# Optimization experiments

Measured on AMD Instinct MI355X. Metric: run time of the kernel, lower is better.

## Reference

```python
import jax, jax.numpy as jnp
import numpy as np

NEG_SLOPE = 0.2  # PyG GATConv default leaky_relu slope
EPS = 1e-16


def gat_conv(x, src, dst, W, att_src, att_dst, bias, heads, concat):
    """PyG-style GATConv. x: [N, Fin]; W: [Fin, heads*C]; att_*: [heads, C].
    Edge (src j -> dst i): alpha_ij = softmax_i(leaky_relu(a_src.h_j + a_dst.h_i)).
    """
    N = x.shape[0]
    h = (x @ W).reshape(N, heads, -1)                       # [N, H, C]
    a_s = jnp.einsum('nhc,hc->nh', h, att_src)              # [N, H]
    a_d = jnp.einsum('nhc,hc->nh', h, att_dst)              # [N, H]
    e = jax.nn.leaky_relu(a_s[src] + a_d[dst], NEG_SLOPE)   # [E, H]
    # numerically stable segment softmax over incoming edges of each dst node
    e_max = jax.ops.segment_max(e, dst, num_segments=N)     # [N, H]
    e_max = jnp.where(jnp.isfinite(e_max), e_max, 0.0)      # isolated nodes
    ex = jnp.exp(e - e_max[dst])                            # [E, H]
    denom = jax.ops.segment_sum(ex, dst, num_segments=N)    # [N, H]
    alpha = ex / (denom[dst] + EPS)                         # [E, H]
    msg = alpha[:, :, None] * h[src]                        # [E, H, C]
    out = jax.ops.segment_sum(msg, dst, num_segments=N)     # [N, H, C]
    out = out.reshape(N, -1) if concat else out.mean(axis=1)
    return out + bias


def setup_inputs() -> dict:
    key = jax.random.key(0)
    ks = jax.random.split(key, 12)
    N, E = 100000, 1600000
    Fin, hidden, heads, Fout = 128, 128, 8, 64
    C1 = hidden // heads  # 16
    s = lambda f: 1.0 / np.sqrt(f)
    x = jax.random.normal(ks[0], (N, Fin), dtype=jnp.float32)
    edge_index = jax.random.randint(ks[1], (2, E), 0, N, dtype=jnp.int64)
    W1 = jax.random.normal(ks[2], (Fin, heads * C1), dtype=jnp.float32) * s(Fin)
    att_src1 = jax.random.normal(ks[3], (heads, C1), dtype=jnp.float32) * s(C1)
    att_dst1 = jax.random.normal(ks[4], (heads, C1), dtype=jnp.float32) * s(C1)
    b1 = jnp.zeros((hidden,), dtype=jnp.float32)
    W2 = jax.random.normal(ks[5], (hidden, Fout), dtype=jnp.float32) * s(hidden)
    att_src2 = jax.random.normal(ks[6], (1, Fout), dtype=jnp.float32) * s(Fout)
    att_dst2 = jax.random.normal(ks[7], (1, Fout), dtype=jnp.float32) * s(Fout)
    b2 = jnp.zeros((Fout,), dtype=jnp.float32)
    return {"x": x, "edge_index": edge_index,
            "W1": W1, "att_src1": att_src1, "att_dst1": att_dst1, "b1": b1,
            "W2": W2, "att_src2": att_src2, "att_dst2": att_dst2, "b2": b2}


def reference(x, edge_index, W1, att_src1, att_dst1, b1, W2, att_src2, att_dst2, b2):
    # eval mode: dropouts are identity
    src, dst = edge_index[0], edge_index[1]
    h = gat_conv(x, src, dst, W1, att_src1, att_dst1, b1, heads=8, concat=True)
    h = jax.nn.elu(h)
    out = gat_conv(h, src, dst, W2, att_src2, att_dst2, b2, heads=1, concat=False)
    return out
```

## Files before the change

### kernel.cpp

```cpp
#include <hip/hip_runtime.h>
#include <hip/hip_bf16.h>
#include <hip/hip_fp16.h>
#include <stdint.h>

#define SLOPE 0.2f
#define EPSV 1e-16f
#define LOG2E 1.44269504f
#define H1W 72
#define H2W 36

#define NPB   512
#define NBMAX 256
#define NBLK1 256

typedef __attribute__((ext_vector_type(8))) short bf16x8;
typedef __attribute__((ext_vector_type(4))) float f32x4;

static __device__ __forceinline__ uint32_t cvtpk(float a, float b) {
    uint32_t r;
    asm("v_cvt_pk_bf16_f32 %0, %1, %2" : "=v"(r) : "v"(a), "v"(b));
    return r;
}
static __device__ __forceinline__ float lof(uint32_t u) { return __uint_as_float(u << 16); }
static __device__ __forceinline__ float hif(uint32_t u) { return __uint_as_float(u & 0xffff0000u); }

static __device__ __forceinline__ uint32_t pkf16(float a, float b) {
    auto r = __builtin_amdgcn_cvt_pkrtz(a, b);
    return __builtin_bit_cast(uint32_t, r);
}

static __device__ __forceinline__ void fmix_lo(float& acc, uint32_t h2, float w) {
    asm("v_fma_mix_f32 %0, %1, %2, %0 op_sel_hi:[1,0,0]" : "+v"(acc) : "v"(h2), "v"(w));
}
static __device__ __forceinline__ void fmix_hi(float& acc, uint32_t h2, float w) {
    asm("v_fma_mix_f32 %0, %1, %2, %0 op_sel:[1,0,0] op_sel_hi:[1,0,0]" : "+v"(acc) : "v"(h2), "v"(w));
}

union FragCvt { uint4 u; bf16x8 f; };

__global__ __launch_bounds__(256) void prep_kernel(
    const float* __restrict__ W1, const float* __restrict__ W2,
    uint32_t* __restrict__ wt1hi, uint32_t* __restrict__ wt1lo,
    uint32_t* __restrict__ wt2hi, uint32_t* __restrict__ wt2lo)
{
    int t = threadIdx.x;
    if (blockIdx.x == 0) {
        for (int i = t; i < 128 * 64; i += 256) {
            int n = i >> 6, kp = i & 63;
            float w0 = W1[(2 * kp) * 128 + n], w1 = W1[(2 * kp + 1) * 128 + n];
            uint32_t h = cvtpk(w0, w1);
            wt1hi[n * 64 + kp] = h;
            wt1lo[n * 64 + kp] = cvtpk(w0 - lof(h), w1 - hif(h));
        }
    } else {
        for (int i = t; i < 64 * 64; i += 256) {
            int n = i >> 6, kp = i & 63;
            float w0 = W2[(2 * kp) * 64 + n], w1 = W2[(2 * kp + 1) * 64 + n];
            uint32_t h = cvtpk(w0, w1);
            wt2hi[n * 64 + kp] = h;
            wt2lo[n * 64 + kp] = cvtpk(w0 - lof(h), w1 - hif(h));
        }
    }
}

__global__ __launch_bounds__(256) void gemm1_mfma(
    const float* __restrict__ x,
    const uint32_t* __restrict__ wthi, const uint32_t* __restrict__ wtlo,
    const float* __restrict__ att_src, const float* __restrict__ att_dst,
    uint32_t* __restrict__ h1p, float* __restrict__ ad1, int N)
{
    __shared__ uint32_t lds[2][128 * 36];
    const int t = threadIdx.x;
    const int w = t >> 6, l = t & 63;
    const int cl = l & 15, rg = l >> 4;
    const int rowbase = blockIdx.x * 128 + w * 32;

    f32x4 zero = {0.f, 0.f, 0.f, 0.f};
    f32x4 acc[2][8];
    #pragma unroll
    for (int rt = 0; rt < 2; ++rt)
        #pragma unroll
        for (int tl = 0; tl < 8; ++tl) acc[rt][tl] = zero;

    for (int kh = 0; kh < 2; ++kh) {
        if (kh) __syncthreads();
        for (int i = t; i < 1024; i += 256) {
            int col = i >> 3, q = i & 7;
            *(uint4*)&lds[0][col * 36 + q * 4] = *(const uint4*)&wthi[col * 64 + kh * 32 + q * 4];
            *(uint4*)&lds[1][col * 36 + q * 4] = *(const uint4*)&wtlo[col * 64 + kh * 32 + q * 4];
        }
        __syncthreads();
        #pragma unroll
        for (int ks = 0; ks < 2; ++ks) {
            const int kg = kh * 64 + ks * 32 + rg * 8;
            bf16x8 ahi[2], alo[2];
            #pragma unroll
            for (int rt = 0; rt < 2; ++rt) {
                int row = rowbase + rt * 16 + cl;
                row = min(row, N - 1);
                const float* xr = x + (size_t)row * 128 + kg;
                float4 v0 = *(const float4*)xr;
                float4 v1 = *(const float4*)(xr + 4);
                uint32_t h0 = cvtpk(v0.x, v0.y), h1 = cvtpk(v0.z, v0.w);
                uint32_t h2 = cvtpk(v1.x, v1.y), h3 = cvtpk(v1.z, v1.w);
                uint32_t l0 = cvtpk(v0.x - lof(h0), v0.y - hif(h0));
                uint32_t l1 = cvtpk(v0.z - lof(h1), v0.w - hif(h1));
                uint32_t l2 = cvtpk(v1.x - lof(h2), v1.y - hif(h2));
                uint32_t l3 = cvtpk(v1.z - lof(h3), v1.w - hif(h3));
                FragCvt ch, clo;
                ch.u  = make_uint4(h0, h1, h2, h3);
                clo.u = make_uint4(l0, l1, l2, l3);
                ahi[rt] = ch.f; alo[rt] = clo.f;
            }
            #pragma unroll
            for (int tl = 0; tl < 8; ++tl) {
                const int off = (tl * 16 + cl) * 36 + ks * 16 + rg * 4;
                bf16x8 bhi = *(const bf16x8*)&lds[0][off];
                bf16x8 blo = *(const bf16x8*)&lds[1][off];
                #pragma unroll
                for (int rt = 0; rt < 2; ++rt) {
                    acc[rt][tl] = __builtin_amdgcn_mfma_f32_16x16x32_bf16(alo[rt], bhi, acc[rt][tl], 0, 0, 0);
                    acc[rt][tl] = __builtin_amdgcn_mfma_f32_16x16x32_bf16(ahi[rt], blo, acc[rt][tl], 0, 0, 0);
                    acc[rt][tl] = __builtin_amdgcn_mfma_f32_16x16x32_bf16(ahi[rt], bhi, acc[rt][tl], 0, 0, 0);
                }
            }
        }
    }

    #pragma unroll
    for (int rt = 0; rt < 2; ++rt) {
        const int rowb = rowbase + rt * 16 + rg * 4;
        #pragma unroll
        for (int tl = 0; tl < 8; ++tl) {
            f32x4 a = acc[rt][tl];
            float as_ = att_src[tl * 16 + cl] * LOG2E, ad_ = att_dst[tl * 16 + cl] * LOG2E;
            float s0 = a.x * as_, s1 = a.y * as_, s2 = a.z * as_, s3 = a.w * as_;
            float d0 = a.x * ad_, d1 = a.y * ad_, d2 = a.z * ad_, d3 = a.w * ad_;
            #pragma unroll
            for (int off = 1; off < 16; off <<= 1) {
                s0 += __shfl_xor(s0, off); s1 += __shfl_xor(s1, off);
                s2 += __shfl_xor(s2, off); s3 += __shfl_xor(s3, off);
                d0 += __shfl_xor(d0, off); d1 += __shfl_xor(d1, off);
                d2 += __shfl_xor(d2, off); d3 += __shfl_xor(d3, off);
            }
            float av[4] = {a.x, a.y, a.z, a.w};
            #pragma unroll
            for (int r = 0; r < 4; ++r) {
                float partner = __shfl_xor(av[r], 1);
                if (!(cl & 1)) {
                    int row = rowb + r;
                    if (row < N)
                        h1p[(size_t)row * H1W + tl * 8 + (cl >> 1)] = pkf16(av[r], partner);
                }
            }
            if (cl == 0) {
                float sv[4] = {s0, s1, s2, s3}, dv[4] = {d0, d1, d2, d3};
                #pragma unroll
                for (int r = 0; r < 4; ++r) {
                    int row = rowb + r;
                    if (row < N) {
                        h1p[(size_t)row * H1W + 64 + tl] = __float_as_uint(sv[r]);
                        ad1[row * 8 + tl] = dv[r];
                    }
                }
            }
        }
    }
}

__global__ __launch_bounds__(256) void gemm2_mfma(
    const float* __restrict__ h,
    const uint32_t* __restrict__ wthi, const uint32_t* __restrict__ wtlo,
    const float* __restrict__ att_src, const float* __restrict__ att_dst,
    uint32_t* __restrict__ h2p, float* __restrict__ ad2, int N)
{
    __shared__ uint32_t lds[2][64 * 36];
    const int t = threadIdx.x;
    const int w = t >> 6, l = t & 63;
    const int cl = l & 15, rg = l >> 4;
    const int rowbase = blockIdx.x * 128 + w * 32;

    f32x4 zero = {0.f, 0.f, 0.f, 0.f};
    f32x4 acc[2][4];
    #pragma unroll
    for (int rt = 0; rt < 2; ++rt)
        #pragma unroll
        for (int tl = 0; tl < 4; ++tl) acc[rt][tl] = zero;

    for (int kh = 0; kh < 2; ++kh) {
        if (kh) __syncthreads();
        for (int i = t; i < 512; i += 256) {
            int col = i >> 3, q = i & 7;
            *(uint4*)&lds[0][col * 36 + q * 4] = *(const uint4*)&wthi[col * 64 + kh * 32 + q * 4];
            *(uint4*)&lds[1][col * 36 + q * 4] = *(const uint4*)&wtlo[col * 64 + kh * 32 + q * 4];
        }
        __syncthreads();
        #pragma unroll
        for (int ks = 0; ks < 2; ++ks) {
            const int kg = kh * 64 + ks * 32 + rg * 8;
            bf16x8 ahi[2], alo[2];
            #pragma unroll
            for (int rt = 0; rt < 2; ++rt) {
                int row = rowbase + rt * 16 + cl;
                row = min(row, N - 1);
                const float* xr = h + (size_t)row * 128 + kg;
                float4 v0 = *(const float4*)xr;
                float4 v1 = *(const float4*)(xr + 4);
                uint32_t h0 = cvtpk(v0.x, v0.y), h1 = cvtpk(v0.z, v0.w);
                uint32_t h2 = cvtpk(v1.x, v1.y), h3 = cvtpk(v1.z, v1.w);
                uint32_t l0 = cvtpk(v0.x - lof(h0), v0.y - hif(h0));
                uint32_t l1 = cvtpk(v0.z - lof(h1), v0.w - hif(h1));
                uint32_t l2 = cvtpk(v1.x - lof(h2), v1.y - hif(h2));
                uint32_t l3 = cvtpk(v1.z - lof(h3), v1.w - hif(h3));
                FragCvt ch, clo;
                ch.u  = make_uint4(h0, h1, h2, h3);
                clo.u = make_uint4(l0, l1, l2, l3);
                ahi[rt] = ch.f; alo[rt] = clo.f;
            }
            #pragma unroll
            for (int tl = 0; tl < 4; ++tl) {
                const int off = (tl * 16 + cl) * 36 + ks * 16 + rg * 4;
                bf16x8 bhi = *(const bf16x8*)&lds[0][off];
                bf16x8 blo = *(const bf16x8*)&lds[1][off];
                #pragma unroll
                for (int rt = 0; rt < 2; ++rt) {
                    acc[rt][tl] = __builtin_amdgcn_mfma_f32_16x16x32_bf16(alo[rt], bhi, acc[rt][tl], 0, 0, 0);
                    acc[rt][tl] = __builtin_amdgcn_mfma_f32_16x16x32_bf16(ahi[rt], blo, acc[rt][tl], 0, 0, 0);
                    acc[rt][tl] = __builtin_amdgcn_mfma_f32_16x16x32_bf16(ahi[rt], bhi, acc[rt][tl], 0, 0, 0);
                }
            }
        }
    }

    #pragma unroll
    for (int rt = 0; rt < 2; ++rt) {
        const int rowb = rowbase + rt * 16 + rg * 4;
        float s0 = 0.f, s1 = 0.f, s2 = 0.f, s3 = 0.f;
        float d0 = 0.f, d1 = 0.f, d2 = 0.f, d3 = 0.f;
        #pragma unroll
        for (int tl = 0; tl < 4; ++tl) {
            f32x4 a = acc[rt][tl];
            float as_ = att_src[tl * 16 + cl] * LOG2E, ad_ = att_dst[tl * 16 + cl] * LOG2E;
            s0 += a.x * as_; s1 += a.y * as_; s2 += a.z * as_; s3 += a.w * as_;
            d0 += a.x * ad_; d1 += a.y * ad_; d2 += a.z * ad_; d3 += a.w * ad_;
            float av[4] = {a.x, a.y, a.z, a.w};
            #pragma unroll
            for (int r = 0; r < 4; ++r) {
                float partner = __shfl_xor(av[r], 1);
                if (!(cl & 1)) {
                    int row = rowb + r;
                    if (row < N)
                        h2p[(size_t)row * H2W + tl * 8 + (cl >> 1)] = pkf16(av[r], partner);
                }
            }
        }
        #pragma unroll
        for (int off = 1; off < 16; off <<= 1) {
            s0 += __shfl_xor(s0, off); s1 += __shfl_xor(s1, off);
            s2 += __shfl_xor(s2, off); s3 += __shfl_xor(s3, off);
            d0 += __shfl_xor(d0, off); d1 += __shfl_xor(d1, off);
            d2 += __shfl_xor(d2, off); d3 += __shfl_xor(d3, off);
        }
        if (cl == 0) {
            float sv[4] = {s0, s1, s2, s3}, dv[4] = {d0, d1, d2, d3};
            #pragma unroll
            for (int r = 0; r < 4; ++r) {
                int row = rowb + r;
                if (row < N) {
                    h2p[(size_t)row * H2W + 32] = __float_as_uint(sv[r]);
                    ad2[row] = dv[r];
                }
            }
        }
    }
}

__global__ __launch_bounds__(256) void p1_count_kernel(
    const int* __restrict__ ei, int* __restrict__ pbh, int E, int NB, int chunk)
{
    __shared__ int hist[NBMAX];
    int t = threadIdx.x;
    if (t < NB) hist[t] = 0;
    __syncthreads();
    int e0 = blockIdx.x * chunk;
    int e1 = min(E, e0 + chunk);
    for (int e = e0 + t; e < e1; e += 256)
        atomicAdd(&hist[ei[E + e] >> 9], 1);
    __syncthreads();
    if (t < NB) pbh[t * NBLK1 + blockIdx.x] = hist[t];
}

__global__ __launch_bounds__(256) void p1_scan_kernel(
    int* __restrict__ pbh, int* __restrict__ bucket_base, int NB, int E)
{
    __shared__ int ps[256];
    int t = threadIdx.x;
    int s = 0;
    if (t < NB) {
        const int* row = &pbh[t * NBLK1];
        for (int b = 0; b < NBLK1; ++b) s += row[b];
    }
    ps[t] = s; __syncthreads();
    for (int off = 1; off < 256; off <<= 1) {
        int add = (t >= off) ? ps[t - off] : 0;
        __syncthreads();
        ps[t] += add;
        __syncthreads();
    }
    int base = ps[t] - s;
    if (t < NB) {
        bucket_base[t] = base;
        int* row = &pbh[t * NBLK1];
        int run = base;
        for (int b = 0; b < NBLK1; ++b) {
            int c = row[b];
            row[b] = run;
            run += c;
        }
    }
    if (t == 0) bucket_base[NB] = E;
}

__global__ __launch_bounds__(256) void p1_place_kernel(
    const int* __restrict__ ei, const int* __restrict__ pbh,
    uint32_t* __restrict__ staging, int E, int NB, int chunk)
{
    __shared__ int lcur[NBMAX];
    int t = threadIdx.x;
    if (t < NB) lcur[t] = pbh[t * NBLK1 + blockIdx.x];
    __syncthreads();
    int e0 = blockIdx.x * chunk;
    int e1 = min(E, e0 + chunk);
    for (int e = e0 + t; e < e1; e += 256) {
        int s = ei[e], d = ei[E + e];
        int b = d >> 9;
        int p = atomicAdd(&lcur[b], 1);
        staging[p] = ((uint32_t)s << 9) | (uint32_t)(d & 511);
    }
}

__global__ __launch_bounds__(256) void p2_build_kernel(
    const uint32_t* __restrict__ staging, const int* __restrict__ bucket_base,
    int* __restrict__ row_start, int* __restrict__ sorted_src, int N, int E, int NB)
{
    __shared__ int cnt[NPB];
    __shared__ int ofs[NPB];
    __shared__ int ps[256];
    int b = blockIdx.x, t = threadIdx.x;
    int base = bucket_base[b], end = bucket_base[b + 1];
    cnt[t] = 0; cnt[t + 256] = 0;
    __syncthreads();
    for (int i = base + t; i < end; i += 256)
        atomicAdd(&cnt[staging[i] & 511], 1);
    __syncthreads();
    int c0 = cnt[2 * t], c1 = cnt[2 * t + 1];
    int p = c0 + c1;
    ps[t] = p; __syncthreads();
    for (int off = 1; off < 256; off <<= 1) {
        int add = (t >= off) ? ps[t - off] : 0;
        __syncthreads();
        ps[t] += add;
        __syncthreads();
    }
    int pex = ps[t] - p;
    ofs[2 * t] = pex;
    ofs[2 * t + 1] = pex + c0;
    __syncthreads();
    int node0 = b * NPB;
    #pragma unroll
    for (int i = t; i < NPB; i += 256) {
        int node = node0 + i;
        if (node < N) row_start[node] = base + ofs[i];
    }
    if (b == NB - 1 && t == 0) row_start[N] = E;
    __syncthreads();
    for (int i = base + t; i < end; i += 256) {
        uint32_t v = staging[i];
        int nl = v & 511;
        int pos = base + atomicAdd(&ofs[nl], 1);
        sorted_src[pos] = (int)(v >> 9);
    }
}

__global__ __launch_bounds__(256) void gather1_kernel(
    const int* __restrict__ row_start, const int* __restrict__ sorted_src,
    const float* __restrict__ ad1, const uint32_t* __restrict__ h1p,
    const float* __restrict__ b1, float* __restrict__ hbuf, int N)
{
    int node = blockIdx.x * 4 + (threadIdx.x >> 6);
    if (node >= N) return;
    const int l  = threadIdx.x & 63;
    const int wh = l & 7;
    const int eA = l >> 3;
    const int c8 = l & 15;
    const int q  = l >> 4;
    const int hB = c8 >> 1;

    int r0 = row_start[node], r1 = row_start[node + 1];

    if (r0 == r1) {
        if (l < 16) {
            #pragma unroll
            for (int g = 0; g < 2; ++g) {
                float4 bv = *(const float4*)&b1[c8 * 8 + g * 4];
                bv.x = bv.x > 0.f ? bv.x : expm1f(bv.x);
                bv.y = bv.y > 0.f ? bv.y : expm1f(bv.y);
                bv.z = bv.z > 0.f ? bv.z : expm1f(bv.z);
                bv.w = bv.w > 0.f ? bv.w : expm1f(bv.w);
                *(float4*)&hbuf[(size_t)node * 128 + c8 * 8 + g * 4] = bv;
            }
        }
        return;
    }

    float adw = ad1[node * 8 + wh];
    const uint32_t* rowp = h1p + 4 * c8;
    float acc[8] = {0.f, 0.f, 0.f, 0.f, 0.f, 0.f, 0.f, 0.f};
    float den = 0.f;

    int jw = r0 + eA;
    int sw0 = sorted_src[jw < r1 ? jw : r0] * H1W;
    int j1 = r0 + 8 + eA;
    int sw1 = sorted_src[j1 < r1 ? j1 : r0] * H1W;
    float av0 = __uint_as_float(h1p[sw0 + 64 + wh]);

    for (int j = r0; j < r1; j += 8) {
        int jn = j + 16 + eA;
        int swn = sorted_src[jn < r1 ? jn : r0] * H1W;
        float avn = __uint_as_float(h1p[sw1 + 64 + wh]);

        float ev = av0 + adw;
        ev = ev > 0.f ? ev : SLOPE * ev;
        float w = (j + eA) < r1 ? exp2f(ev) : 0.f;
        den += w;

        #pragma unroll
        for (int k = 0; k < 2; ++k) {
            int eidx = q + 4 * k;
            float wk  = __shfl(w,   eidx * 8 + hB, 64);
            int   ofk = __shfl(sw0, eidx * 8,      64);
            uint4 hv = *(const uint4*)(rowp + ofk);
            fmix_lo(acc[0], hv.x, wk); fmix_hi(acc[1], hv.x, wk);
            fmix_lo(acc[2], hv.y, wk); fmix_hi(acc[3], hv.y, wk);
            fmix_lo(acc[4], hv.z, wk); fmix_hi(acc[5], hv.z, wk);
            fmix_lo(acc[6], hv.w, wk); fmix_hi(acc[7], hv.w, wk);
        }
        sw0 = sw1; sw1 = swn; av0 = avn;
    }

    den += __shfl_xor(den, 8, 64);
    den += __shfl_xor(den, 16, 64);
    den += __shfl_xor(den, 32, 64);
    float dB = __shfl(den, hB, 64);

    #pragma unroll
    for (int i = 0; i < 8; ++i) {
        acc[i] += __shfl_xor(acc[i], 16, 64);
        acc[i] += __shfl_xor(acc[i], 32, 64);
    }

    if (l < 16) {
        float inv = 1.0f / (dB + EPSV);
        #pragma unroll
        for (int g = 0; g < 2; ++g) {
            float4 bv = *(const float4*)&b1[c8 * 8 + g * 4];
            float v0 = acc[g * 4 + 0] * inv + bv.x;
            float v1 = acc[g * 4 + 1] * inv + bv.y;
            float v2 = acc[g * 4 + 2] * inv + bv.z;
            float v3 = acc[g * 4 + 3] * inv + bv.w;
            v0 = v0 > 0.f ? v0 : expm1f(v0);
            v1 = v1 > 0.f ? v1 : expm1f(v1);
            v2 = v2 > 0.f ? v2 : expm1f(v2);
            v3 = v3 > 0.f ? v3 : expm1f(v3);
            *(float4*)&hbuf[(size_t)node * 128 + c8 * 8 + g * 4] = make_float4(v0, v1, v2, v3);
        }
    }
}

__global__ __launch_bounds__(256) void gather2_kernel(
    const int* __restrict__ row_start, const int* __restrict__ sorted_src,
    const float* __restrict__ ad2, const uint32_t* __restrict__ h2p,
    const float* __restrict__ b2, float* __restrict__ out, int N)
{
    int node = blockIdx.x * 8 + (threadIdx.x >> 5);
    if (node >= N) return;
    const int l  = threadIdx.x & 31;
    const int eA = l & 7;
    const int c8 = l & 7;
    const int q  = l >> 3;

    int r0 = row_start[node], r1 = row_start[node + 1];

    if (r0 == r1) {
        if (l < 8) {
            #pragma unroll
            for (int g = 0; g < 2; ++g) {
                float4 bv = *(const float4*)&b2[c8 * 8 + g * 4];
                *(float4*)&out[(size_t)node * 64 + c8 * 8 + g * 4] = bv;
            }
        }
        return;
    }

    float ad = ad2[node];
    const uint32_t* rowp = h2p + 4 * c8;
    float acc[8] = {0.f, 0.f, 0.f, 0.f, 0.f, 0.f, 0.f, 0.f};
    float den = 0.f;

    int jw = r0 + eA;
    int sw0 = sorted_src[jw < r1 ? jw : r0] * H2W;
    int j1 = r0 + 8 + eA;
    int sw1 = sorted_src[j1 < r1 ? j1 : r0] * H2W;
    float av0 = __uint_as_float(h2p[sw0 + 32]);

    for (int j = r0; j < r1; j += 8) {
        int jn = j + 16 + eA;
        int swn = sorted_src[jn < r1 ? jn : r0] * H2W;
        float avn = __uint_as_float(h2p[sw1 + 32]);

        float ev = av0 + ad;
        ev = ev > 0.f ? ev : SLOPE * ev;
        float w = (j + eA) < r1 ? exp2f(ev) : 0.f;
        den += w;

        #pragma unroll
        for (int k = 0; k < 2; ++k) {
            int eidx = q + 4 * k;
            float wk  = __shfl(w,   eidx, 32);
            int   ofk = __shfl(sw0, eidx, 32);
            uint4 hv = *(const uint4*)(rowp + ofk);
            fmix_lo(acc[0], hv.x, wk); fmix_hi(acc[1], hv.x, wk);
            fmix_lo(acc[2], hv.y, wk); fmix_hi(acc[3], hv.y, wk);
            fmix_lo(acc[4], hv.z, wk); fmix_hi(acc[5], hv.z, wk);
            fmix_lo(acc[6], hv.w, wk); fmix_hi(acc[7], hv.w, wk);
        }
        sw0 = sw1; sw1 = swn; av0 = avn;
    }

    den += __shfl_xor(den, 1, 32);
    den += __shfl_xor(den, 2, 32);
    den += __shfl_xor(den, 4, 32);
    #pragma unroll
    for (int i = 0; i < 8; ++i) {
        acc[i] += __shfl_xor(acc[i], 8, 32);
        acc[i] += __shfl_xor(acc[i], 16, 32);
    }

    if (l < 8) {
        float inv = 1.0f / (den + EPSV);
        #pragma unroll
        for (int g = 0; g < 2; ++g) {
            float4 bv = *(const float4*)&b2[c8 * 8 + g * 4];
            *(float4*)&out[(size_t)node * 64 + c8 * 8 + g * 4] =
                make_float4(acc[g * 4 + 0] * inv + bv.x, acc[g * 4 + 1] * inv + bv.y,
                            acc[g * 4 + 2] * inv + bv.z, acc[g * 4 + 3] * inv + bv.w);
        }
    }
}

extern "C" void kernel_launch(void* const* d_in, const int* in_sizes, int n_in,
                              void* d_out, int out_size, void* d_ws, size_t ws_size,
                              hipStream_t stream)
{
    const int N = in_sizes[0] / 128;
    const int E = in_sizes[1] / 2;
    const int NB = (N + NPB - 1) / NPB;
    const int chunk = (E + NBLK1 - 1) / NBLK1;

    const float* x        = (const float*)d_in[0];
    const int*   ei       = (const int*)  d_in[1];
    const float* W1       = (const float*)d_in[2];
    const float* att_src1 = (const float*)d_in[3];
    const float* att_dst1 = (const float*)d_in[4];
    const float* b1       = (const float*)d_in[5];
    const float* W2       = (const float*)d_in[6];
    const float* att_src2 = (const float*)d_in[7];
    const float* att_dst2 = (const float*)d_in[8];
    const float* b2       = (const float*)d_in[9];
    float* out = (float*)d_out;

    uint32_t* h1p  = (uint32_t*)d_ws;
    float* hbuf    = (float*)(h1p + (size_t)N * H1W);
    float* ad1     = hbuf + (size_t)N * 128;
    float* ad2     = ad1  + (size_t)N * 8;
    int* row_start   = (int*)(ad2 + N);
    int* bucket_base = row_start + (N + 1);
    int* pbh         = bucket_base + (NB + 1);
    int* sorted_src  = pbh + NB * NBLK1;
    uint32_t* staging = (uint32_t*)(sorted_src + E);
    uint32_t* wt1hi = staging + E;
    uint32_t* wt1lo = wt1hi + 128 * 64;
    uint32_t* wt2hi = wt1lo + 128 * 64;
    uint32_t* wt2lo = wt2hi + 64 * 64;
    uint32_t* h2p   = h1p;

    prep_kernel<<<2, 256, 0, stream>>>(W1, W2, wt1hi, wt1lo, wt2hi, wt2lo);

    p1_count_kernel<<<NBLK1, 256, 0, stream>>>(ei, pbh, E, NB, chunk);
    p1_scan_kernel <<<1, 256, 0, stream>>>(pbh, bucket_base, NB, E);
    p1_place_kernel<<<NBLK1, 256, 0, stream>>>(ei, pbh, staging, E, NB, chunk);
    p2_build_kernel<<<NB, 256, 0, stream>>>(staging, bucket_base, row_start, sorted_src, N, E, NB);

    gemm1_mfma<<<(N + 127) / 128, 256, 0, stream>>>(x, wt1hi, wt1lo, att_src1, att_dst1, h1p, ad1, N);
    gather1_kernel<<<(N + 3) / 4, 256, 0, stream>>>(row_start, sorted_src, ad1, h1p, b1, hbuf, N);

    gemm2_mfma<<<(N + 127) / 128, 256, 0, stream>>>(hbuf, wt2hi, wt2lo, att_src2, att_dst2, h2p, ad2, N);
    gather2_kernel<<<(N + 7) / 8, 256, 0, stream>>>(row_start, sorted_src, ad2, h2p, b2, out, N);
}
```

Measured before the change: 282.9 us.

## Parallelize CSR bucket scan across blocks and use finer buckets

```diff
diff --git a/kernel.cpp b/kernel.cpp
--- a/kernel.cpp
+++ b/kernel.cpp
@@ -9,9 +9,8 @@
 #define H1W 72
 #define H2W 36
 
-#define NPB   512
-#define NBMAX 256
-#define NBLK1 256
+#define NPB2  256
+#define NBLK  512
 
 typedef __attribute__((ext_vector_type(8))) short bf16x8;
 typedef __attribute__((ext_vector_type(4))) float f32x4;
@@ -275,110 +274,120 @@
     }
 }
 
-__global__ __launch_bounds__(256) void p1_count_kernel(
+__global__ __launch_bounds__(256) void s_count(
     const int* __restrict__ ei, int* __restrict__ pbh, int E, int NB, int chunk)
 {
-    __shared__ int hist[NBMAX];
+    __shared__ int hist[512];
     int t = threadIdx.x;
-    if (t < NB) hist[t] = 0;
+    hist[t] = 0; hist[t + 256] = 0;
     __syncthreads();
-    int e0 = blockIdx.x * chunk;
-    int e1 = min(E, e0 + chunk);
+    int e0 = blockIdx.x * chunk, e1 = min(E, e0 + chunk);
     for (int e = e0 + t; e < e1; e += 256)
-        atomicAdd(&hist[ei[E + e] >> 9], 1);
+        atomicAdd(&hist[ei[E + e] >> 8], 1);
     __syncthreads();
-    if (t < NB) pbh[t * NBLK1 + blockIdx.x] = hist[t];
-}
-
-__global__ __launch_bounds__(256) void p1_scan_kernel(
-    int* __restrict__ pbh, int* __restrict__ bucket_base, int NB, int E)
+    for (int b = t; b < NB; b += 256)
+        pbh[(size_t)b * NBLK + blockIdx.x] = hist[b];
+}
+
+__global__ __launch_bounds__(256) void s_scanA(
+    const int* __restrict__ pbh, int* __restrict__ btot, int NB)
+{
+    __shared__ int red[256];
+    int b = blockIdx.x, t = threadIdx.x;
+    int s = pbh[(size_t)b * NBLK + t] + pbh[(size_t)b * NBLK + 256 + t];
+    red[t] = s; __syncthreads();
+    for (int off = 128; off; off >>= 1) {
+        if (t < off) red[t] += red[t + off];
+        __syncthreads();
+    }
+    if (t == 0) btot[b] = red[0];
+}
+
+__global__ __launch_bounds__(512) void s_scanB(
+    const int* __restrict__ btot, int* __restrict__ bucket_base, int NB, int E)
+{
+    __shared__ int sc[512];
+    int t = threadIdx.x;
+    int v = (t < NB) ? btot[t] : 0;
+    sc[t] = v; __syncthreads();
+    for (int off = 1; off < 512; off <<= 1) {
+        int add = (t >= off) ? sc[t - off] : 0;
+        __syncthreads();
+        sc[t] += add;
+        __syncthreads();
+    }
+    if (t < NB) bucket_base[t] = sc[t] - v;
+    if (t == 0) bucket_base[NB] = E;
+}
+
+__global__ __launch_bounds__(256) void s_scanC(
+    int* __restrict__ pbh, const int* __restrict__ bucket_base, int NB)
 {
     __shared__ int ps[256];
-    int t = threadIdx.x;
-    int s = 0;
-    if (t < NB) {
-        const int* row = &pbh[t * NBLK1];
-        for (int b = 0; b < NBLK1; ++b) s += row[b];
-    }
-    ps[t] = s; __syncthreads();
+    int b = blockIdx.x, t = threadIdx.x;
+    int v0 = pbh[(size_t)b * NBLK + 2 * t], v1 = pbh[(size_t)b * NBLK + 2 * t + 1];
+    int p = v0 + v1;
+    ps[t] = p; __syncthreads();
     for (int off = 1; off < 256; off <<= 1) {
         int add = (t >= off) ? ps[t - off] : 0;
         __syncthreads();
         ps[t] += add;
         __syncthreads();
     }
-    int base = ps[t] - s;
-    if (t < NB) {
-        bucket_base[t] = base;
-        int* row = &pbh[t * NBLK1];
-        int run = base;
-        for (int b = 0; b < NBLK1; ++b) {
-            int c = row[b];
-            row[b] = run;
-            run += c;
-        }
-    }
-    if (t == 0) bucket_base[NB] = E;
-}
-
-__global__ __launch_bounds__(256) void p1_place_kernel(
+    int ex = bucket_base[b] + ps[t] - p;
+    pbh[(size_t)b * NBLK + 2 * t]     = ex;
+    pbh[(size_t)b * NBLK + 2 * t + 1] = ex + v0;
+}
+
+__global__ __launch_bounds__(256) void s_place(
     const int* __restrict__ ei, const int* __restrict__ pbh,
     uint32_t* __restrict__ staging, int E, int NB, int chunk)
 {
-    __shared__ int lcur[NBMAX];
+    __shared__ int lcur[512];
     int t = threadIdx.x;
-    if (t < NB) lcur[t] = pbh[t * NBLK1 + blockIdx.x];
+    if (t < NB)       lcur[t]       = pbh[(size_t)t * NBLK + blockIdx.x];
+    if (t + 256 < NB) lcur[t + 256] = pbh[(size_t)(t + 256) * NBLK + blockIdx.x];
     __syncthreads();
-    int e0 = blockIdx.x * chunk;
-    int e1 = min(E, e0 + chunk);
+    int e0 = blockIdx.x * chunk, e1 = min(E, e0 + chunk);
     for (int e = e0 + t; e < e1; e += 256) {
         int s = ei[e], d = ei[E + e];
-        int b = d >> 9;
-        int p = atomicAdd(&lcur[b], 1);
-        staging[p] = ((uint32_t)s << 9) | (uint32_t)(d & 511);
-    }
-}
-
-__global__ __launch_bounds__(256) void p2_build_kernel(
+        int p = atomicAdd(&lcur[d >> 8], 1);
+        staging[p] = ((uint32_t)s << 8) | (uint32_t)(d & 255);
+    }
+}
+
+__global__ __launch_bounds__(256) void s_build(
     const uint32_t* __restrict__ staging, const int* __restrict__ bucket_base,
     int* __restrict__ row_start, int* __restrict__ sorted_src, int N, int E, int NB)
 {
-    __shared__ int cnt[NPB];
-    __shared__ int ofs[NPB];
+    __shared__ int cnt[256];
+    __shared__ int ofs[256];
     __shared__ int ps[256];
     int b = blockIdx.x, t = threadIdx.x;
     int base = bucket_base[b], end = bucket_base[b + 1];
-    cnt[t] = 0; cnt[t + 256] = 0;
+    cnt[t] = 0;
     __syncthreads();
     for (int i = base + t; i < end; i += 256)
-        atomicAdd(&cnt[staging[i] & 511], 1);
+        atomicAdd(&cnt[staging[i] & 255], 1);
     __syncthreads();
-    int c0 = cnt[2 * t], c1 = cnt[2 * t + 1];
-    int p = c0 + c1;
-    ps[t] = p; __syncthreads();
+    int c = cnt[t];
+    ps[t] = c; __syncthreads();
     for (int off = 1; off < 256; off <<= 1) {
         int add = (t >= off) ? ps[t - off] : 0;
         __syncthreads();
         ps[t] += add;
         __syncthreads();
     }
-    int pex = ps[t] - p;
-    ofs[2 * t] = pex;
-    ofs[2 * t + 1] = pex + c0;
-    __syncthreads();
-    int node0 = b * NPB;
-    #pragma unroll
-    for (int i = t; i < NPB; i += 256) {
-        int node = node0 + i;
-        if (node < N) row_start[node] = base + ofs[i];
-    }
+    int ex = ps[t] - c;
+    ofs[t] = ex;
+    int node = b * NPB2 + t;
+    if (node < N) row_start[node] = base + ex;
     if (b == NB - 1 && t == 0) row_start[N] = E;
     __syncthreads();
     for (int i = base + t; i < end; i += 256) {
         uint32_t v = staging[i];
-        int nl = v & 511;
-        int pos = base + atomicAdd(&ofs[nl], 1);
-        sorted_src[pos] = (int)(v >> 9);
+        int pos = base + atomicAdd(&ofs[v & 255], 1);
+        sorted_src[pos] = (int)(v >> 8);
     }
 }
 
@@ -564,8 +573,8 @@
 {
     const int N = in_sizes[0] / 128;
     const int E = in_sizes[1] / 2;
-    const int NB = (N + NPB - 1) / NPB;
-    const int chunk = (E + NBLK1 - 1) / NBLK1;
+    const int NB = (N + NPB2 - 1) / NPB2;
+    const int chunk = (E + NBLK - 1) / NBLK;
 
     const float* x        = (const float*)d_in[0];
     const int*   ei       = (const int*)  d_in[1];
@@ -585,8 +594,9 @@
     float* ad2     = ad1  + (size_t)N * 8;
     int* row_start   = (int*)(ad2 + N);
     int* bucket_base = row_start + (N + 1);
-    int* pbh         = bucket_base + (NB + 1);
-    int* sorted_src  = pbh + NB * NBLK1;
+    int* btot        = bucket_base + (NB + 1);
+    int* pbh         = btot + NB;
+    int* sorted_src  = pbh + (size_t)NB * NBLK;
     uint32_t* staging = (uint32_t*)(sorted_src + E);
     uint32_t* wt1hi = staging + E;
     uint32_t* wt1lo = wt1hi + 128 * 64;
@@ -596,10 +606,12 @@
 
     prep_kernel<<<2, 256, 0, stream>>>(W1, W2, wt1hi, wt1lo, wt2hi, wt2lo);
 
-    p1_count_kernel<<<NBLK1, 256, 0, stream>>>(ei, pbh, E, NB, chunk);
-    p1_scan_kernel <<<1, 256, 0, stream>>>(pbh, bucket_base, NB, E);
-    p1_place_kernel<<<NBLK1, 256, 0, stream>>>(ei, pbh, staging, E, NB, chunk);
-    p2_build_kernel<<<NB, 256, 0, stream>>>(staging, bucket_base, row_start, sorted_src, N, E, NB);
+    s_count<<<NBLK, 256, 0, stream>>>(ei, pbh, E, NB, chunk);
+    s_scanA<<<NB, 256, 0, stream>>>(pbh, btot, NB);
+    s_scanB<<<1, 512, 0, stream>>>(btot, bucket_base, NB, E);
+    s_scanC<<<NB, 256, 0, stream>>>(pbh, bucket_base, NB);
+    s_place<<<NBLK, 256, 0, stream>>>(ei, pbh, staging, E, NB, chunk);
+    s_build<<<NB, 256, 0, stream>>>(staging, bucket_base, row_start, sorted_src, N, E, NB);
 
     gemm1_mfma<<<(N + 127) / 128, 256, 0, stream>>>(x, wt1hi, wt1lo, att_src1, att_dst1, h1p, ad1, N);
     gather1_kernel<<<(N + 3) / 4, 256, 0, stream>>>(row_start, sorted_src, ad1, h1p, b1, hbuf, N);
```

Result: faster. 257.9 us (-8.8%).
